# Optimization experiments

Hardware: AMD Instinct MI355X
Metric: run time of the kernel (lower is better)

Reference implementation:

```python
import jax, jax.numpy as jnp
import numpy as np

N = 50000      # nodes
E = 500000     # edges
D_IN = 512
D_H = 512
D_OUT = 256


def setup_inputs() -> dict:
    key = jax.random.key(0)
    ks = jax.random.split(key, 5)
    x = jax.random.normal(ks[0], (N, D_IN), dtype=jnp.float32)
    edge_index = jax.random.randint(ks[1], (2, E), 0, N, dtype=jnp.int32)
    W1 = jax.random.normal(ks[2], (D_IN, D_H), dtype=jnp.float32) / np.float32(np.sqrt(D_IN))
    b1 = jnp.zeros((D_H,), dtype=jnp.float32)
    W2 = jax.random.normal(ks[3], (D_H, D_OUT), dtype=jnp.float32) / np.float32(np.sqrt(D_H))
    b2 = jnp.zeros((D_OUT,), dtype=jnp.float32)
    return {"x": x, "edge_index": edge_index, "W1": W1, "b1": b1, "W2": W2, "b2": b2}


def _gcn_conv(x, src, dst, W, b, n):
    # PyG GCNConv: h = X W; add self-loops; symmetric norm D^-1/2 (A+I) D^-1/2; aggregate at dst; + bias
    h = x @ W
    loop = jnp.arange(n, dtype=src.dtype)
    src_sl = jnp.concatenate([src, loop])
    dst_sl = jnp.concatenate([dst, loop])
    deg = jax.ops.segment_sum(jnp.ones_like(src_sl, dtype=h.dtype), dst_sl, num_segments=n)
    dinv = jnp.where(deg > 0, jax.lax.rsqrt(deg), 0.0)
    norm = dinv[src_sl] * dinv[dst_sl]                     # [E+N]
    msg = h[src_sl] * norm[:, None]                        # [E+N, out]
    out = jax.ops.segment_sum(msg, dst_sl, num_segments=n) # [N, out]
    return out + b


def reference(x, edge_index, W1, b1, W2, b2):
    # Encoder.forward in eval mode (dropout = identity, bn='none' = identity), ELU activation after each conv.
    src, dst = edge_index[0], edge_index[1]
    h = _gcn_conv(x, src, dst, W1, b1, N)
    h = jax.nn.elu(h)
    h = _gcn_conv(h, src, dst, W2, b2, N)
    return jax.nn.elu(h)
```

## Files before the change

kernel.cpp:

```cpp
#include <hip/hip_runtime.h>
#include <math.h>

#define N_NODES 50000
#define N_EDGES 500000
#define D_IN 512
#define D_H  512
#define D_OUT 256
#define NB 196
#define NBK 1954

typedef __attribute__((ext_vector_type(8))) short bf16x8;
typedef __attribute__((ext_vector_type(8))) unsigned short ushort8;
typedef __attribute__((ext_vector_type(4))) float f32x4;

__device__ __forceinline__ float b2f(unsigned short u) {
    union { unsigned int i; float f; } v; v.i = ((unsigned int)u) << 16; return v.f;
}
__device__ __forceinline__ unsigned short f2b(float f) {
    unsigned int x = __float_as_uint(f);
    unsigned int r = (x + 0x7fffu + ((x >> 16) & 1u)) >> 16;
    return (unsigned short)r;
}


__global__ __launch_bounds__(256) void k_zero(int* __restrict__ p, int n) {
    int i = blockIdx.x * 256 + threadIdx.x;
    if (i < n) p[i] = 0;
}


#define CB   12500
#define W1B  256
#define W2B  128

__global__ __launch_bounds__(256) void k_prep(const float* __restrict__ x,
                                              unsigned short* __restrict__ xb,
                                              const float* __restrict__ W1,
                                              unsigned short* __restrict__ W1t,
                                              const float* __restrict__ W2,
                                              unsigned short* __restrict__ W2t,
                                              const int* __restrict__ dst,
                                              int* __restrict__ indeg) {
    __shared__ float t[32][33];
    int b = blockIdx.x;
    const int tid = threadIdx.x;

    if (b < NBK) {
        const int e = b * 256 + tid;
        if (e < N_EDGES) atomicAdd(&indeg[dst[e]], 1);
        return;
    }
    b -= NBK;
    if (b < CB) {
        const long long i = (long long)b * 256 + tid;
        float4 v0 = ((const float4*)x)[i * 2];
        float4 v1 = ((const float4*)x)[i * 2 + 1];
        ushort8 o;
        o[0] = f2b(v0.x); o[1] = f2b(v0.y); o[2] = f2b(v0.z); o[3] = f2b(v0.w);
        o[4] = f2b(v1.x); o[5] = f2b(v1.y); o[6] = f2b(v1.z); o[7] = f2b(v1.w);
        ((ushort8*)xb)[i] = o;
        return;
    }
    b -= CB;
    const float* W;
    unsigned short* Wt;
    int K, N, idx;
    if (b < W1B) { W = W1; Wt = W1t; K = D_IN; N = D_H; idx = b; }
    else         { W = W2; Wt = W2t; K = D_H; N = D_OUT; idx = b - W1B; }
    const int nkb = K / 32;
    const int bk = (idx % nkb) * 32;
    const int bn = (idx / nkb) * 32;
    const int tx = tid & 31, ty = tid >> 5;
    for (int i = ty; i < 32; i += 8) t[i][tx] = W[(size_t)(bk + i) * N + bn + tx];
    __syncthreads();
    for (int i = ty; i < 32; i += 8)
        Wt[(size_t)(bn + i) * K + bk + tx] = f2b(t[tx][i]);
}


__global__ __launch_bounds__(256) void k_partials(const int* __restrict__ indeg,
                                                  int* __restrict__ bsum) {
    __shared__ int wsum[4];
    const int tid = threadIdx.x, lane = tid & 63, w = tid >> 6;
    const int i = blockIdx.x * 256 + tid;
    int v = (i < N_NODES) ? indeg[i] : 0;
#pragma unroll
    for (int o = 32; o > 0; o >>= 1) v += __shfl_down(v, o, 64);
    if (lane == 0) wsum[w] = v;
    __syncthreads();
    if (tid == 0) bsum[blockIdx.x] = wsum[0] + wsum[1] + wsum[2] + wsum[3];
}

__global__ __launch_bounds__(256) void k_scanb(const int* __restrict__ bsum,
                                               int* __restrict__ boff) {
    __shared__ int wsum[4];
    const int tid = threadIdx.x, lane = tid & 63, w = tid >> 6;
    const int v = (tid < NB) ? bsum[tid] : 0;
    int s = v;
#pragma unroll
    for (int o = 1; o < 64; o <<= 1) {
        int t = __shfl_up(s, o, 64);
        if (lane >= o) s += t;
    }
    if (lane == 63) wsum[w] = s;
    __syncthreads();
    int add = 0;
    for (int k = 0; k < w; ++k) add += wsum[k];
    if (tid < NB) boff[tid] = add + s - v;
}

__global__ __launch_bounds__(256) void k_finalize(const int* __restrict__ indeg,
                                                  const int* __restrict__ boff,
                                                  int* __restrict__ row_start,
                                                  int* __restrict__ cursor,
                                                  float* __restrict__ dinv) {
    __shared__ int wsum[4];
    const int tid = threadIdx.x, lane = tid & 63, w = tid >> 6;
    const int i = blockIdx.x * 256 + tid;
    const int v = (i < N_NODES) ? indeg[i] : 0;
    int s = v;
#pragma unroll
    for (int o = 1; o < 64; o <<= 1) {
        int t = __shfl_up(s, o, 64);
        if (lane >= o) s += t;
    }
    if (lane == 63) wsum[w] = s;
    __syncthreads();
    int add = boff[blockIdx.x];
    for (int k = 0; k < w; ++k) add += wsum[k];
    if (i < N_NODES) {
        const int excl = add + s - v;
        row_start[i] = excl;
        cursor[i] = excl;
        dinv[i] = rsqrtf((float)(1 + v));
    }
    if (i == N_NODES) row_start[N_NODES] = N_EDGES;
}


__device__ __forceinline__ void gload16(const void* g, void* l) {
    __builtin_amdgcn_global_load_lds(
        (const __attribute__((address_space(1))) unsigned int*)g,
        (__attribute__((address_space(3))) unsigned int*)l, 16, 0, 0);
}

template <bool FUSE_BUCKET>
__global__ __launch_bounds__(256, 4) void k_gemm(const unsigned short* __restrict__ A,
                                                 const unsigned short* __restrict__ Bt,
                                                 unsigned short* __restrict__ C,
                                                 const float* __restrict__ rowscale,
                                                 int M, int N, int K,
                                                 int ncb, int nrb,
                                                 const int* __restrict__ src,
                                                 const int* __restrict__ dst,
                                                 int* __restrict__ cursor,
                                                 int* __restrict__ csr_src) {
    __shared__ __align__(16) short lds[16384];

    if (FUSE_BUCKET && blockIdx.x < NBK) {
        const int e = blockIdx.x * 256 + threadIdx.x;
        if (e < N_EDGES) {
            const int pos = atomicAdd(&cursor[dst[e]], 1);
            csr_src[pos] = src[e];
        }
        return;
    }
    const int bid = blockIdx.x - (FUSE_BUCKET ? NBK : 0);
    const int xcd = bid & 7;
    const int sidx = bid >> 3;
    const int cb = sidx % ncb;
    const int rb = (sidx / ncb) * 8 + xcd;
    if (rb >= nrb) return;
    const int brow = rb * 128;
    const int bcol = cb * 128;

    const int tid = threadIdx.x;
    const int wid = tid >> 6;
    const int lane = tid & 63;
    const int wr = wid >> 1, wc = wid & 1;
    const int lhi = lane >> 4, llo = lane & 15;

    f32x4 acc[4][4];
#pragma unroll
    for (int i = 0; i < 4; ++i)
#pragma unroll
        for (int j = 0; j < 4; ++j) acc[i][j] = (f32x4){0.f, 0.f, 0.f, 0.f};

#define STAGE(buf, kt)                                                          \
    {                                                                           \
        _Pragma("unroll") for (int g = 0; g < 2; ++g) {                         \
            const int s = g * 256 + tid;                                        \
            const int row = s >> 2;                                             \
            const int sc = (s & 3) ^ (row & 3);                                 \
            int gr = brow + row; gr = gr < M ? gr : M - 1;                      \
            gload16(A + (size_t)gr * K + (kt) + sc * 8,                         \
                    &lds[(buf) * 4096 + (g * 256 + wid * 64) * 8]);             \
            gload16(Bt + (size_t)(bcol + row) * K + (kt) + sc * 8,              \
                    &lds[8192 + (buf) * 4096 + (g * 256 + wid * 64) * 8]);      \
        }                                                                       \
    }

    const int nt = K / 32;

    STAGE(0, 0);
    __syncthreads();

    int cur = 0;
    for (int t = 0; t < nt; ++t) {
        if (t + 1 < nt) STAGE(cur ^ 1, (t + 1) * 32);

        bf16x8 af[4], bf[4];
#pragma unroll
        for (int mi = 0; mi < 4; ++mi) {
            const int row = wr * 64 + mi * 16 + llo;
            af[mi] = *(const bf16x8*)&lds[cur * 4096 + row * 32 + ((lhi ^ (row & 3)) * 8)];
        }
#pragma unroll
        for (int ni = 0; ni < 4; ++ni) {
            const int row = wc * 64 + ni * 16 + llo;
            bf[ni] = *(const bf16x8*)&lds[8192 + cur * 4096 + row * 32 + ((lhi ^ (row & 3)) * 8)];
        }
#pragma unroll
        for (int mi = 0; mi < 4; ++mi)
#pragma unroll
            for (int ni = 0; ni < 4; ++ni)
                acc[mi][ni] = __builtin_amdgcn_mfma_f32_16x16x32_bf16(
                    af[mi], bf[ni], acc[mi][ni], 0, 0, 0);

        __syncthreads();
        cur ^= 1;
    }
#undef STAGE

    short* cws = &lds[wid * 4096];

#pragma unroll
    for (int mi = 0; mi < 4; ++mi) {
#pragma unroll
        for (int r = 0; r < 4; ++r) {
            const int lrow = mi * 16 + lhi * 4 + r;
            int grow = brow + wr * 64 + lrow;
            grow = grow < M ? grow : M - 1;
            const float ds = rowscale[grow];
#pragma unroll
            for (int ni = 0; ni < 4; ++ni) {
                const int col = ni * 16 + llo;
                const int chunk = (col >> 3) ^ (lrow & 7);
                cws[lrow * 64 + chunk * 8 + (col & 7)] = (short)f2b(acc[mi][ni][r] * ds);
            }
        }
    }
    __syncthreads();

    {
        const int rsub = lane >> 3;
        const int c = lane & 7;
#pragma unroll
        for (int i = 0; i < 8; ++i) {
            const int row = i * 8 + rsub;
            const ushort8 o = *(const ushort8*)&cws[row * 64 + ((c ^ (row & 7)) * 8)];
            const int grow = brow + wr * 64 + row;
            if (grow < M)
                *(ushort8*)(C + (size_t)grow * N + bcol + wc * 64 + c * 8) = o;
        }
    }
}


template <int D, bool BF16_OUT>
__global__ __launch_bounds__(256) void k_aggregate(const unsigned short* __restrict__ H,
                                                   const float* __restrict__ bias,
                                                   void* __restrict__ outv,
                                                   const int* __restrict__ row_start,
                                                   const int* __restrict__ csr_src,
                                                   const float* __restrict__ dinv) {
    const int wid = threadIdx.x >> 6;
    const int lane = threadIdx.x & 63;
    int n, c0;
    if (D == 512) { n = blockIdx.x * 4 + wid; c0 = lane * 8; }
    else          { n = blockIdx.x * 8 + wid * 2 + (lane >> 5); c0 = (lane & 31) * 8; }
    if (n >= N_NODES) return;

    float acc[8];
    {
        ushort8 v = *(const ushort8*)(H + (size_t)n * D + c0);
#pragma unroll
        for (int e = 0; e < 8; ++e) acc[e] = b2f(v[e]);
    }

    const int e0 = row_start[n];
    const int e1 = row_start[n + 1];
    int j = e0;
    for (; j + 8 <= e1; j += 8) {
        int s[8];
#pragma unroll
        for (int q = 0; q < 8; ++q) s[q] = csr_src[j + q];
#pragma unroll
        for (int h = 0; h < 2; ++h) {
            const ushort8 v0 = *(const ushort8*)(H + (size_t)s[h * 4 + 0] * D + c0);
            const ushort8 v1 = *(const ushort8*)(H + (size_t)s[h * 4 + 1] * D + c0);
            const ushort8 v2 = *(const ushort8*)(H + (size_t)s[h * 4 + 2] * D + c0);
            const ushort8 v3 = *(const ushort8*)(H + (size_t)s[h * 4 + 3] * D + c0);
#pragma unroll
            for (int e = 0; e < 8; ++e) {
                acc[e] += b2f(v0[e]);
                acc[e] += b2f(v1[e]);
                acc[e] += b2f(v2[e]);
                acc[e] += b2f(v3[e]);
            }
        }
    }
    for (; j + 4 <= e1; j += 4) {
        const int s0 = csr_src[j + 0];
        const int s1 = csr_src[j + 1];
        const int s2 = csr_src[j + 2];
        const int s3 = csr_src[j + 3];
        const ushort8 v0 = *(const ushort8*)(H + (size_t)s0 * D + c0);
        const ushort8 v1 = *(const ushort8*)(H + (size_t)s1 * D + c0);
        const ushort8 v2 = *(const ushort8*)(H + (size_t)s2 * D + c0);
        const ushort8 v3 = *(const ushort8*)(H + (size_t)s3 * D + c0);
#pragma unroll
        for (int e = 0; e < 8; ++e) {
            acc[e] += b2f(v0[e]);
            acc[e] += b2f(v1[e]);
            acc[e] += b2f(v2[e]);
            acc[e] += b2f(v3[e]);
        }
    }
    for (; j < e1; ++j) {
        const int s = csr_src[j];
        const ushort8 v = *(const ushort8*)(H + (size_t)s * D + c0);
#pragma unroll
        for (int e = 0; e < 8; ++e) acc[e] += b2f(v[e]);
    }

    const float di = dinv[n];
#pragma unroll
    for (int e = 0; e < 8; ++e) {
        float t = fmaf(acc[e], di, bias[c0 + e]);
        acc[e] = t > 0.f ? t : expf(t) - 1.f;
    }

    if (BF16_OUT) {
        ushort8 o;
#pragma unroll
        for (int e = 0; e < 8; ++e) o[e] = f2b(acc[e]);
        *(ushort8*)((unsigned short*)outv + (size_t)n * D + c0) = o;
    } else {
        float* orow = (float*)outv + (size_t)n * D + c0;
        *(float4*)orow = make_float4(acc[0], acc[1], acc[2], acc[3]);
        *(float4*)(orow + 4) = make_float4(acc[4], acc[5], acc[6], acc[7]);
    }
}


extern "C" void kernel_launch(void* const* d_in, const int* in_sizes, int n_in,
                              void* d_out, int out_size, void* d_ws, size_t ws_size,
                              hipStream_t stream) {
    const float* x  = (const float*)d_in[0];
    const int* ei   = (const int*)d_in[1];
    const int* src  = ei;
    const int* dst  = ei + N_EDGES;
    const float* W1 = (const float*)d_in[2];
    const float* b1 = (const float*)d_in[3];
    const float* W2 = (const float*)d_in[4];
    const float* b2 = (const float*)d_in[5];
    float* out = (float*)d_out;

    char* ws = (char*)d_ws;
    size_t off = 0;
    auto alloc = [&](size_t bytes) -> void* {
        void* p = ws + off;
        off = (off + bytes + 255) & ~(size_t)255;
        return p;
    };
    int*   indeg     = (int*)alloc((size_t)N_NODES * 4);
    int*   bsum      = (int*)alloc((size_t)NB * 4);
    int*   boff      = (int*)alloc((size_t)NB * 4);
    int*   row_start = (int*)alloc((size_t)(N_NODES + 1) * 4);
    int*   cursor    = (int*)alloc((size_t)N_NODES * 4);
    int*   csr_src   = (int*)alloc((size_t)N_EDGES * 4);
    float* dinv      = (float*)alloc((size_t)N_NODES * 4);
    unsigned short* W1t  = (unsigned short*)alloc((size_t)D_H * D_IN * 2);
    unsigned short* W2t  = (unsigned short*)alloc((size_t)D_OUT * D_H * 2);
    unsigned short* xb   = (unsigned short*)alloc((size_t)N_NODES * D_IN * 2);
    unsigned short* H1   = (unsigned short*)alloc((size_t)N_NODES * D_H * 2);
    unsigned short* out1 = (unsigned short*)alloc((size_t)N_NODES * D_H * 2);
    unsigned short* H2   = (unsigned short*)alloc((size_t)N_NODES * D_OUT * 2);

    k_zero<<<NB, 256, 0, stream>>>(indeg, N_NODES);
    k_prep<<<NBK + CB + W1B + W2B, 256, 0, stream>>>(x, xb, W1, W1t, W2, W2t, dst, indeg);
    k_partials<<<NB, 256, 0, stream>>>(indeg, bsum);
    k_scanb<<<1, 256, 0, stream>>>(bsum, boff);
    k_finalize<<<NB, 256, 0, stream>>>(indeg, boff, row_start, cursor, dinv);

    const int nrb = (N_NODES + 127) / 128;
    const int rgrp = (nrb + 7) / 8;

    {
        const int ncb = D_H / 128;
        k_gemm<true><<<NBK + 8 * ncb * rgrp, 256, 0, stream>>>(
            xb, W1t, H1, dinv, N_NODES, D_H, D_IN, ncb, nrb, src, dst, cursor, csr_src);
    }
    k_aggregate<512, true><<<(N_NODES + 3) / 4, 256, 0, stream>>>(H1, b1, out1, row_start, csr_src, dinv);

    {
        const int ncb = D_OUT / 128;
        k_gemm<false><<<8 * ncb * rgrp, 256, 0, stream>>>(
            out1, W2t, H2, dinv, N_NODES, D_OUT, D_H, ncb, nrb, nullptr, nullptr, nullptr, nullptr);
    }
    k_aggregate<256, false><<<(N_NODES + 7) / 8, 256, 0, stream>>>(H2, b2, out, row_start, csr_src, dinv);
}
```

Baseline: 272.8 us.

## Fuse fp32-to-bf16 conversion of x into first GEMM's A-tile loading

Removes the separate pass that converted the fp32 node features to bf16 in the prep kernel. The first GEMM now loads fp32 A tiles into registers, converts them to bf16 and writes them to LDS after the MFMA work of each step. This avoids writing and re-reading a bf16 copy of x, but every column block now reads the larger fp32 tile. A also moves from async global-to-LDS loads to register staging, which raises register pressure.

After: 270.4 us. About the same (-0.9%).

```diff
diff --git a/kernel.cpp b/kernel.cpp
--- a/kernel.cpp
+++ b/kernel.cpp
@@ -29,13 +29,10 @@
 }
 
 
-#define CB   12500
 #define W1B  256
 #define W2B  128
 
-__global__ __launch_bounds__(256) void k_prep(const float* __restrict__ x,
-                                              unsigned short* __restrict__ xb,
-                                              const float* __restrict__ W1,
+__global__ __launch_bounds__(256) void k_prep(const float* __restrict__ W1,
                                               unsigned short* __restrict__ W1t,
                                               const float* __restrict__ W2,
                                               unsigned short* __restrict__ W2t,
@@ -51,17 +48,6 @@
         return;
     }
     b -= NBK;
-    if (b < CB) {
-        const long long i = (long long)b * 256 + tid;
-        float4 v0 = ((const float4*)x)[i * 2];
-        float4 v1 = ((const float4*)x)[i * 2 + 1];
-        ushort8 o;
-        o[0] = f2b(v0.x); o[1] = f2b(v0.y); o[2] = f2b(v0.z); o[3] = f2b(v0.w);
-        o[4] = f2b(v1.x); o[5] = f2b(v1.y); o[6] = f2b(v1.z); o[7] = f2b(v1.w);
-        ((ushort8*)xb)[i] = o;
-        return;
-    }
-    b -= CB;
     const float* W;
     unsigned short* Wt;
     int K, N, idx;
@@ -144,8 +130,8 @@
         (__attribute__((address_space(3))) unsigned int*)l, 16, 0, 0);
 }
 
-template <bool FUSE_BUCKET>
-__global__ __launch_bounds__(256, 4) void k_gemm(const unsigned short* __restrict__ A,
+template <bool A32, bool FUSE_BUCKET>
+__global__ __launch_bounds__(256, 4) void k_gemm(const void* __restrict__ Av,
                                                  const unsigned short* __restrict__ Bt,
                                                  unsigned short* __restrict__ C,
                                                  const float* __restrict__ rowscale,
@@ -180,34 +166,85 @@
     const int wr = wid >> 1, wc = wid & 1;
     const int lhi = lane >> 4, llo = lane & 15;
 
+    const float* Af = (const float*)Av;
+    const unsigned short* Ab = (const unsigned short*)Av;
+
     f32x4 acc[4][4];
 #pragma unroll
     for (int i = 0; i < 4; ++i)
 #pragma unroll
         for (int j = 0; j < 4; ++j) acc[i][j] = (f32x4){0.f, 0.f, 0.f, 0.f};
 
-#define STAGE(buf, kt)                                                          \
+    float4 ar[2][2];
+
+#define STAGE_A16(buf, kt)                                                      \
     {                                                                           \
         _Pragma("unroll") for (int g = 0; g < 2; ++g) {                         \
             const int s = g * 256 + tid;                                        \
             const int row = s >> 2;                                             \
             const int sc = (s & 3) ^ (row & 3);                                 \
             int gr = brow + row; gr = gr < M ? gr : M - 1;                      \
-            gload16(A + (size_t)gr * K + (kt) + sc * 8,                         \
+            gload16(Ab + (size_t)gr * K + (kt) + sc * 8,                        \
                     &lds[(buf) * 4096 + (g * 256 + wid * 64) * 8]);             \
+        }                                                                       \
+    }
+#define STAGE_B(buf, kt)                                                        \
+    {                                                                           \
+        _Pragma("unroll") for (int g = 0; g < 2; ++g) {                         \
+            const int s = g * 256 + tid;                                        \
+            const int row = s >> 2;                                             \
+            const int sc = (s & 3) ^ (row & 3);                                 \
             gload16(Bt + (size_t)(bcol + row) * K + (kt) + sc * 8,              \
                     &lds[8192 + (buf) * 4096 + (g * 256 + wid * 64) * 8]);      \
         }                                                                       \
     }
+#define LOAD_A32(kt)                                                            \
+    {                                                                           \
+        _Pragma("unroll") for (int g = 0; g < 2; ++g) {                         \
+            const int s = g * 256 + tid;                                        \
+            const int row = s >> 2;                                             \
+            const int sc = (s & 3) ^ (row & 3);                                 \
+            int gr = brow + row; gr = gr < M ? gr : M - 1;                      \
+            const float* p = Af + (size_t)gr * K + (kt) + sc * 8;               \
+            ar[g][0] = *(const float4*)p;                                       \
+            ar[g][1] = *(const float4*)(p + 4);                                 \
+        }                                                                       \
+    }
+#define WRITE_A32(buf)                                                          \
+    {                                                                           \
+        _Pragma("unroll") for (int g = 0; g < 2; ++g) {                         \
+            ushort8 u;                                                          \
+            u[0] = f2b(ar[g][0].x); u[1] = f2b(ar[g][0].y);                     \
+            u[2] = f2b(ar[g][0].z); u[3] = f2b(ar[g][0].w);                     \
+            u[4] = f2b(ar[g][1].x); u[5] = f2b(ar[g][1].y);                     \
+            u[6] = f2b(ar[g][1].z); u[7] = f2b(ar[g][1].w);                     \
+            *(ushort8*)&lds[(buf) * 4096 + (g * 256 + tid) * 8] = u;            \
+        }                                                                       \
+    }
 
     const int nt = K / 32;
 
-    STAGE(0, 0);
+    if (A32) {
+        LOAD_A32(0);
+        STAGE_B(0, 0);
+        WRITE_A32(0);
+    } else {
+        STAGE_A16(0, 0);
+        STAGE_B(0, 0);
+    }
     __syncthreads();
 
     int cur = 0;
     for (int t = 0; t < nt; ++t) {
-        if (t + 1 < nt) STAGE(cur ^ 1, (t + 1) * 32);
+        const bool more = (t + 1 < nt);
+        if (more) {
+            if (A32) {
+                LOAD_A32((t + 1) * 32);
+            } else {
+                STAGE_A16(cur ^ 1, (t + 1) * 32);
+            }
+            STAGE_B(cur ^ 1, (t + 1) * 32);
+        }
 
         bf16x8 af[4], bf[4];
 #pragma unroll
@@ -227,10 +264,15 @@
                 acc[mi][ni] = __builtin_amdgcn_mfma_f32_16x16x32_bf16(
                     af[mi], bf[ni], acc[mi][ni], 0, 0, 0);
 
+        if (A32 && more) WRITE_A32(cur ^ 1);
+
         __syncthreads();
         cur ^= 1;
     }
-#undef STAGE
+#undef STAGE_A16
+#undef STAGE_B
+#undef LOAD_A32
+#undef WRITE_A32
 
     short* cws = &lds[wid * 4096];
 
@@ -383,13 +425,12 @@
     float* dinv      = (float*)alloc((size_t)N_NODES * 4);
     unsigned short* W1t  = (unsigned short*)alloc((size_t)D_H * D_IN * 2);
     unsigned short* W2t  = (unsigned short*)alloc((size_t)D_OUT * D_H * 2);
-    unsigned short* xb   = (unsigned short*)alloc((size_t)N_NODES * D_IN * 2);
     unsigned short* H1   = (unsigned short*)alloc((size_t)N_NODES * D_H * 2);
     unsigned short* out1 = (unsigned short*)alloc((size_t)N_NODES * D_H * 2);
     unsigned short* H2   = (unsigned short*)alloc((size_t)N_NODES * D_OUT * 2);
 
     k_zero<<<NB, 256, 0, stream>>>(indeg, N_NODES);
-    k_prep<<<NBK + CB + W1B + W2B, 256, 0, stream>>>(x, xb, W1, W1t, W2, W2t, dst, indeg);
+    k_prep<<<NBK + W1B + W2B, 256, 0, stream>>>(W1, W1t, W2, W2t, dst, indeg);
     k_partials<<<NB, 256, 0, stream>>>(indeg, bsum);
     k_scanb<<<1, 256, 0, stream>>>(bsum, boff);
     k_finalize<<<NB, 256, 0, stream>>>(indeg, boff, row_start, cursor, dinv);
@@ -399,14 +440,14 @@
 
     {
         const int ncb = D_H / 128;
-        k_gemm<true><<<NBK + 8 * ncb * rgrp, 256, 0, stream>>>(
-            xb, W1t, H1, dinv, N_NODES, D_H, D_IN, ncb, nrb, src, dst, cursor, csr_src);
+        k_gemm<true, true><<<NBK + 8 * ncb * rgrp, 256, 0, stream>>>(
+            x, W1t, H1, dinv, N_NODES, D_H, D_IN, ncb, nrb, src, dst, cursor, csr_src);
     }
     k_aggregate<512, true><<<(N_NODES + 3) / 4, 256, 0, stream>>>(H1, b1, out1, row_start, csr_src, dinv);
 
     {
         const int ncb = D_OUT / 128;
-        k_gemm<false><<<8 * ncb * rgrp, 256, 0, stream>>>(
+        k_gemm<false, false><<<8 * ncb * rgrp, 256, 0, stream>>>(
             out1, W2t, H2, dinv, N_NODES, D_OUT, D_H, ncb, nrb, nullptr, nullptr, nullptr, nullptr);
     }
     k_aggregate<256, false><<<(N_NODES + 7) / 8, 256, 0, stream>>>(H2, b2, out, row_start, csr_src, dinv);
```

## Triple-buffer GEMM LDS staging with explicit vmcnt waits and new swizzle

Applied to the files above, without the earlier changes.

The bf16 MFMA GEMM now uses three LDS buffers per operand instead of two, prefetching two k-tiles ahead. It replaces __syncthreads with manual s_waitcnt vmcnt plus s_barrier so more global loads stay in flight. The LDS swizzle changes to XOR on (row>>1)&3 to cut bank conflicts. Separately, the zeroing kernel becomes hipMemsetAsync. Shared memory grows from 32KB to 48KB per block, which can lower occupancy under launch_bounds(256,4), and the manual waitcnt counts must stay correct.

Result: slower. 281.0 us (+3.0%).

```diff
diff --git a/kernel.cpp b/kernel.cpp
--- a/kernel.cpp
+++ b/kernel.cpp
@@ -20,12 +20,6 @@
     unsigned int x = __float_as_uint(f);
     unsigned int r = (x + 0x7fffu + ((x >> 16) & 1u)) >> 16;
     return (unsigned short)r;
-}
-
-
-__global__ __launch_bounds__(256) void k_zero(int* __restrict__ p, int n) {
-    int i = blockIdx.x * 256 + threadIdx.x;
-    if (i < n) p[i] = 0;
 }
 
 
@@ -155,7 +149,7 @@
                                                  const int* __restrict__ dst,
                                                  int* __restrict__ cursor,
                                                  int* __restrict__ csr_src) {
-    __shared__ __align__(16) short lds[16384];
+    __shared__ __align__(16) short lds[24576];
 
     if (FUSE_BUCKET && blockIdx.x < NBK) {
         const int e = blockIdx.x * 256 + threadIdx.x;
@@ -186,39 +180,42 @@
 #pragma unroll
         for (int j = 0; j < 4; ++j) acc[i][j] = (f32x4){0.f, 0.f, 0.f, 0.f};
 
-#define STAGE(buf, kt)                                                          \
+#define STAGE(bufidx, kt)                                                       \
     {                                                                           \
         _Pragma("unroll") for (int g = 0; g < 2; ++g) {                         \
             const int s = g * 256 + tid;                                        \
             const int row = s >> 2;                                             \
-            const int sc = (s & 3) ^ (row & 3);                                 \
+            const int sc = (s & 3) ^ ((s >> 3) & 3);                            \
             int gr = brow + row; gr = gr < M ? gr : M - 1;                      \
             gload16(A + (size_t)gr * K + (kt) + sc * 8,                         \
-                    &lds[(buf) * 4096 + (g * 256 + wid * 64) * 8]);             \
+                    &lds[(bufidx) * 4096 + (g * 256 + wid * 64) * 8]);          \
             gload16(Bt + (size_t)(bcol + row) * K + (kt) + sc * 8,              \
-                    &lds[8192 + (buf) * 4096 + (g * 256 + wid * 64) * 8]);      \
+                    &lds[12288 + (bufidx) * 4096 + (g * 256 + wid * 64) * 8]);  \
         }                                                                       \
     }
 
     const int nt = K / 32;
 
     STAGE(0, 0);
-    __syncthreads();
-
-    int cur = 0;
+    STAGE(1, 32);
+    asm volatile("s_waitcnt vmcnt(4)" ::: "memory");
+    __builtin_amdgcn_s_barrier();
+    __builtin_amdgcn_sched_barrier(0);
+
+    int b0 = 0, b1 = 1, b2 = 2;
     for (int t = 0; t < nt; ++t) {
-        if (t + 1 < nt) STAGE(cur ^ 1, (t + 1) * 32);
+        if (t + 2 < nt) STAGE(b2, (t + 2) * 32);
 
         bf16x8 af[4], bf[4];
 #pragma unroll
         for (int mi = 0; mi < 4; ++mi) {
             const int row = wr * 64 + mi * 16 + llo;
-            af[mi] = *(const bf16x8*)&lds[cur * 4096 + row * 32 + ((lhi ^ (row & 3)) * 8)];
+            af[mi] = *(const bf16x8*)&lds[b0 * 4096 + row * 32 + ((lhi ^ ((row >> 1) & 3)) * 8)];
         }
 #pragma unroll
         for (int ni = 0; ni < 4; ++ni) {
             const int row = wc * 64 + ni * 16 + llo;
-            bf[ni] = *(const bf16x8*)&lds[8192 + cur * 4096 + row * 32 + ((lhi ^ (row & 3)) * 8)];
+            bf[ni] = *(const bf16x8*)&lds[12288 + b0 * 4096 + row * 32 + ((lhi ^ ((row >> 1) & 3)) * 8)];
         }
 #pragma unroll
         for (int mi = 0; mi < 4; ++mi)
@@ -227,8 +224,15 @@
                 acc[mi][ni] = __builtin_amdgcn_mfma_f32_16x16x32_bf16(
                     af[mi], bf[ni], acc[mi][ni], 0, 0, 0);
 
-        __syncthreads();
-        cur ^= 1;
+        if (t + 2 < nt) {
+            asm volatile("s_waitcnt vmcnt(4)" ::: "memory");
+        } else {
+            asm volatile("s_waitcnt vmcnt(0)" ::: "memory");
+        }
+        __builtin_amdgcn_s_barrier();
+        __builtin_amdgcn_sched_barrier(0);
+
+        const int tmp = b0; b0 = b1; b1 = b2; b2 = tmp;
     }
 #undef STAGE
 
@@ -388,7 +392,7 @@
     unsigned short* out1 = (unsigned short*)alloc((size_t)N_NODES * D_H * 2);
     unsigned short* H2   = (unsigned short*)alloc((size_t)N_NODES * D_OUT * 2);
 
-    k_zero<<<NB, 256, 0, stream>>>(indeg, N_NODES);
+    hipMemsetAsync(indeg, 0, (size_t)N_NODES * 4, stream);
     k_prep<<<NBK + CB + W1B + W2B, 256, 0, stream>>>(x, xb, W1, W1t, W2, W2t, dst, indeg);
     k_partials<<<NB, 256, 0, stream>>>(indeg, bsum);
     k_scanb<<<1, 256, 0, stream>>>(bsum, boff);
```
